# Kernel tuning notes

Hardware: AMD Instinct MI355X
Metric: run time of the kernel (lower is better)

The kernel has to match this reference:

```python
import jax, jax.numpy as jnp
import numpy as np

AMPLITUDE_STD = 4.2  # repo constant (unexported); normalization scale for ln_mag
EPS = 1e-8


def _interp_bias(table, x):
    # Linear interpolation of a 1D table over frequency domain [-1, 1].
    n = table.shape[0]
    idx = jnp.clip((x + 1.0) * 0.5 * (n - 1), 0.0, float(n - 1))
    i0 = jnp.floor(idx).astype(jnp.int32)
    i1 = jnp.minimum(i0 + 1, n - 1)
    w = idx - i0.astype(idx.dtype)
    return table[i0] * (1.0 - w) + table[i1] * w


def setup_inputs() -> dict:
    key = jax.random.key(0)
    k1, k2, k3, k4 = jax.random.split(key, 4)
    B, F, P, W, H = 8, 128, 32, 96, 96
    return {
        "mode_shapes": jax.random.normal(k1, (B, 2, P, W, H), dtype=jnp.float32),
        "mode_responses": jax.random.normal(k2, (B, F, 2, P), dtype=jnp.float32),
        "freqs": jax.random.uniform(k3, (B, F), dtype=jnp.float32, minval=-1.0, maxval=1.0),
        "bias_table": jax.random.normal(k4, (250,), dtype=jnp.float32) * 0.1,
    }


def reference(mode_shapes, mode_responses, freqs, bias_table):
    B, _, P, W, H = mode_shapes.shape
    F = mode_responses.shape[1]
    # _normalize_mode: L2 norm over (real/imag, W, H) per (batch, peak)
    norm = jnp.sqrt(jnp.sum(mode_shapes ** 2, axis=(1, 3, 4)))  # (B,P)
    ms = mode_shapes / (norm[:, None, :, None, None] + EPS)
    s_r, s_i = ms[:, 0], ms[:, 1]                                # (B,P,W,H)
    t_r, t_i = mode_responses[:, :, 0], mode_responses[:, :, 1]  # (B,F,P)
    f = 1.0 / P
    # complex superposition over modes: contraction over n_peaks
    rr = jnp.einsum('bpwh,bfp->bfwh', s_r, t_r)
    ii = jnp.einsum('bpwh,bfp->bfwh', s_i, t_i)
    ri = jnp.einsum('bpwh,bfp->bfwh', s_r, t_i)
    ir = jnp.einsum('bpwh,bfp->bfwh', s_i, t_r)
    r_new = f * (rr - ii)  # (B,F,W,H)
    i_new = f * (ri + ir)
    mag2 = r_new ** 2 + i_new ** 2
    bias = _interp_bias(bias_table, freqs)                       # (B,F)
    ln_mag = (jnp.log(mag2 + EPS) + bias[:, :, None, None]) / AMPLITUDE_STD
    fnorm = jnp.sum(mag2, axis=(-1, -2), keepdims=True)
    fnorm = jnp.sqrt(jnp.clip(fnorm, jnp.finfo(fnorm.dtype).eps))
    normed_field = jnp.stack([r_new / fnorm, i_new / fnorm], axis=2)  # (B,F,2,W,H)
    # aux sparsity loss over mode responses
    mr = mode_responses.reshape(B, F * 2, P)
    aux_sparse = jnp.mean(jnp.mean(jnp.log(jnp.linalg.norm(mr, axis=1) + 1.0), axis=1))
    return ln_mag, normed_field, aux_sparse
```

## Files before the change

kernel.cpp:

```cpp
#include <hip/hip_runtime.h>
#include <hip/hip_bf16.h>
#include <math.h>

#define WHN 9216
#define PN 32
#define FN 128
#define BN 8
#define EPSF 1e-8f
#define INV_STD 0.23809523809f
#define AUX_IDX 28311552

typedef __attribute__((ext_vector_type(8))) short short8;
typedef __attribute__((ext_vector_type(16))) float f32x16;

__device__ __forceinline__ unsigned short bfbits(__hip_bfloat16 h) {
  return *reinterpret_cast<unsigned short*>(&h);
}

__device__ __forceinline__ unsigned int bfsplit_pk(float v) {
  __hip_bfloat16 h = __float2bfloat16(v);
  unsigned int hs = bfbits(h);
  float r = v - __bfloat162float(h);
  unsigned int ls = bfbits(__float2bfloat16(r));
  return hs | (ls << 16);
}

__global__ __launch_bounds__(256) void k_gram(const float* __restrict__ ms,
                                              float* __restrict__ wsM,
                                              float* __restrict__ wsA,
                                              float* __restrict__ part,
                                              int use_part) {
  const int b = blockIdx.y;
  const int chunk = blockIdx.x;
  const int tid = threadIdx.x;
  __shared__ float4 sA[32][32];
  __shared__ float4 sB[32][32];
  __shared__ float pbuf[2][2048];
  const float4* ms4 = (const float4*)ms;
#pragma unroll
  for (int k = 0; k < 4; ++k) {
    int i4 = tid + k * 256;
    int xq = i4 & 31, p = i4 >> 5;
    sA[xq][p ^ xq] = ms4[((b * 2 + 0) * 32 + p) * 2304 + chunk * 32 + xq];
    sB[xq][p ^ xq] = ms4[((b * 2 + 1) * 32 + p) * 2304 + chunk * 32 + xq];
  }
  __syncthreads();
  const int w = tid >> 6, lane = tid & 63;
  const int pg = lane & 7, qg = lane >> 3;
  float accM[4][4] = {{0}}, accA[4][4] = {{0}};
  for (int xq = w; xq < 32; xq += 4) {
    float4 pa[4], pb[4], qa[4], qb[4];
#pragma unroll
    for (int j = 0; j < 4; ++j) {
      pa[j] = sA[xq][(pg + 8 * j) ^ xq];
      pb[j] = sB[xq][(pg + 8 * j) ^ xq];
      qa[j] = sA[xq][(qg + 8 * j) ^ xq];
      qb[j] = sB[xq][(qg + 8 * j) ^ xq];
    }
#pragma unroll
    for (int j = 0; j < 4; ++j)
#pragma unroll
      for (int k = 0; k < 4; ++k) {
        accM[j][k] += pa[j].x * qa[k].x + pb[j].x * qb[k].x
                    + pa[j].y * qa[k].y + pb[j].y * qb[k].y
                    + pa[j].z * qa[k].z + pb[j].z * qb[k].z
                    + pa[j].w * qa[k].w + pb[j].w * qb[k].w;
        accA[j][k] += pa[j].x * qb[k].x - pb[j].x * qa[k].x
                    + pa[j].y * qb[k].y - pb[j].y * qa[k].y
                    + pa[j].z * qb[k].z - pb[j].z * qa[k].z
                    + pa[j].w * qb[k].w - pb[j].w * qa[k].w;
      }
  }
  if (w < 2) {
#pragma unroll
    for (int j = 0; j < 4; ++j)
#pragma unroll
      for (int k = 0; k < 4; ++k) {
        pbuf[w][lane * 32 + j * 4 + k] = accM[j][k];
        pbuf[w][lane * 32 + 16 + j * 4 + k] = accA[j][k];
      }
  }
  __syncthreads();
  if (w >= 2) {
#pragma unroll
    for (int j = 0; j < 4; ++j)
#pragma unroll
      for (int k = 0; k < 4; ++k) {
        pbuf[w - 2][lane * 32 + j * 4 + k] += accM[j][k];
        pbuf[w - 2][lane * 32 + 16 + j * 4 + k] += accA[j][k];
      }
  }
  __syncthreads();
  for (int idx = tid; idx < 2048; idx += 256) {
    float v = pbuf[0][idx] + pbuf[1][idx];
    if (use_part) {
      part[((size_t)(b * 72 + chunk)) * 2048 + idx] = v;
    } else {
      int lane2 = idx >> 5, r = idx & 31;
      int mat = r >> 4, rr = r & 15, j = rr >> 2, k = rr & 3;
      int p = (lane2 & 7) + 8 * j, q = (lane2 >> 3) + 8 * k;
      float* dst = mat ? wsA : wsM;
      atomicAdd(dst + (b << 10) + p * 32 + q, v);
    }
  }
}

__global__ __launch_bounds__(256) void k_mid(const float* __restrict__ part,
                                             float* __restrict__ wsM,
                                             float* __restrict__ wsA,
                                             float* __restrict__ wsc,
                                             float* __restrict__ out) {
  int g = blockIdx.x * 256 + threadIdx.x;
  if (g == 0) out[AUX_IDX] = 0.f;
  int b = g >> 11, idx = g & 2047;
  const float* p = part + ((size_t)b * 72) * 2048 + idx;
  float s = 0.f;
#pragma unroll 8
  for (int c = 0; c < 72; ++c) s += p[(size_t)c * 2048];
  int lane2 = idx >> 5, r = idx & 31;
  int mat = r >> 4, rr = r & 15, j = rr >> 2, k = rr & 3;
  int pp = (lane2 & 7) + 8 * j, q = (lane2 >> 3) + 8 * k;
  (mat ? wsA : wsM)[(b << 10) + pp * 32 + q] = s;
  if (!mat && pp == q) wsc[(b << 5) + pp] = (1.0f / 32.0f) / (sqrtf(s) + EPSF);
}

__global__ void k_cfromM(const float* __restrict__ wsM, float* __restrict__ wsc,
                         float* __restrict__ out) {
  int tid = threadIdx.x;
  if (tid == 0) out[AUX_IDX] = 0.f;
  int b = tid >> 5, p = tid & 31;
  float m = wsM[(b << 10) + p * 33];
  wsc[tid] = (1.0f / 32.0f) / (sqrtf(m) + EPSF);
}

__global__ __launch_bounds__(64) void k_fnb(const float* __restrict__ t,
                                            const float* __restrict__ freqs,
                                            const float* __restrict__ btab,
                                            const float* __restrict__ wsM,
                                            const float* __restrict__ wsA,
                                            const float* __restrict__ wsc,
                                            float* __restrict__ wsinv,
                                            float* __restrict__ wsbias,
                                            short* __restrict__ wsT,
                                            float* __restrict__ out) {
  const int lane = threadIdx.x;
  if (blockIdx.x >= 1032) {
    const int b = blockIdx.x - 1032;
    __shared__ float sc[32];
    if (lane < 32) sc[lane] = wsc[b * 32 + lane];
    __syncthreads();
    short* dstH = wsT + (size_t)b * 16384;
    short* dstL = dstH + 8192;
#pragma unroll 2
    for (int it = 0; it < 16; ++it) {
      int slot = it * 64 + lane;
      int fl = slot >> 3, g = slot & 7;
      const float* src = t + ((size_t)(b * 128 + fl) * 2 + (g >> 2)) * 32 + (g & 3) * 8;
      int gs = g ^ (fl & 7);
      short8 hv, lv;
#pragma unroll
      for (int e = 0; e < 8; ++e) {
        unsigned int pk = bfsplit_pk(src[e] * sc[(g & 3) * 8 + e]);
        hv[e] = (short)(pk & 0xFFFFu);
        lv[e] = (short)(pk >> 16);
      }
      *(short8*)&dstH[fl * 64 + gs * 8] = hv;
      *(short8*)&dstL[fl * 64 + gs * 8] = lv;
    }
    return;
  }
  if (blockIdx.x >= 1024) {
    const int b = blockIdx.x - 1024;
    const int p = lane & 31, comp = lane >> 5;
    float acc = 0.f;
#pragma unroll 4
    for (int f = 0; f < FN; ++f) {
      float v = t[((size_t)(b * FN + f) * 2 + comp) * PN + p];
      acc = fmaf(v, v, acc);
    }
    acc += __shfl_xor(acc, 32);
    float val = logf(sqrtf(acc) + 1.0f);
#pragma unroll
    for (int off = 1; off <= 16; off <<= 1) val += __shfl_xor(val, off);
    if (lane == 0) atomicAdd(out + AUX_IDX, val * (1.0f / 256.0f));
    return;
  }
  const int bf = blockIdx.x;
  const int b = bf >> 7;
  __shared__ float tt[64];
  {
    int p = lane & 31, comp = lane >> 5;
    tt[lane] = t[(bf * 2 + comp) * PN + p] * wsc[(b << 5) + p];
  }
  __syncthreads();
  const int pp = lane & 31, qh = lane >> 5;
  const float* Mrow = wsM + (b << 10) + pp * 32 + qh * 16;
  const float* Arow = wsA + (b << 10) + pp * 32 + qh * 16;
  float ap = tt[pp], bp = tt[32 + pp];
  float S = 0.f;
#pragma unroll
  for (int k = 0; k < 16; ++k) {
    int q = qh * 16 + k;
    float aq = tt[q], bq = tt[32 + q];
    S += (ap * aq + bp * bq) * Mrow[k] + 2.0f * (bp * aq) * Arow[k];
  }
#pragma unroll
  for (int off = 32; off; off >>= 1) S += __shfl_xor(S, off);
  if (lane == 0) {
    float fn = sqrtf(fmaxf(S, 1.1920929e-7f));
    wsinv[bf] = 1.0f / fn;
    float x = freqs[bf];
    float idx = (x + 1.0f) * 0.5f * 249.0f;
    idx = fminf(fmaxf(idx, 0.0f), 249.0f);
    float fi = floorf(idx);
    int i0 = (int)fi;
    int i1 = min(i0 + 1, 249);
    float wvv = idx - fi;
    wsbias[bf] = btab[i0] * (1.0f - wvv) + btab[i1] * wvv;
  }
}

#define MFMA32(A, B, C) __builtin_amdgcn_mfma_f32_32x32x16_bf16(A, B, C, 0, 0, 0)
__global__ __launch_bounds__(256, 2) void k_main(const float* __restrict__ ms,
                                                 const short* __restrict__ wsT,
                                                 const float* __restrict__ wsinv,
                                                 const float* __restrict__ wsbias,
                                                 float* __restrict__ out) {
  __shared__ short tHs[4096];
  __shared__ short tLs[4096];
  __shared__ float sInv[64], sBias[64];
  const int b = blockIdx.y;
  const int z = blockIdx.z;
  const int tid = threadIdx.x;
  const int lane = tid & 63, wv = tid >> 6;
  const int col = lane & 31, hf = lane >> 5;
  const int pix = blockIdx.x * 128 + wv * 32 + col;
  const int f0 = z * 64;

  {
    const short* gH = wsT + (size_t)b * 16384 + (size_t)z * 4096;
#pragma unroll
    for (int it = 0; it < 4; ++it) {
      int chunk = wv * 4 + it;
      int half = chunk >> 3;
      int off = (chunk & 7) * 512;
      const short* g = gH + half * 8192 + off + lane * 8;
      short* l = (half ? tLs : tHs) + off;
      __builtin_amdgcn_global_load_lds(
          (const __attribute__((address_space(1))) unsigned int*)g,
          (__attribute__((address_space(3))) unsigned int*)l, 16, 0, 0);
    }
  }

  const float* msb = ms + (size_t)b * 64 * WHN + pix;
  short8 sHf[4], sLf[4];
#pragma unroll
  for (int kg = 0; kg < 4; ++kg) {
#pragma unroll
    for (int j = 0; j < 8; ++j) {
      int k = kg * 16 + hf * 8 + j;
      unsigned int pk = bfsplit_pk(msb[(size_t)k * WHN]);
      sHf[kg][j] = (short)(pk & 0xFFFFu);
      sLf[kg][j] = (short)(pk >> 16);
    }
  }
  short8 msk;
#pragma unroll
  for (int j = 0; j < 8; ++j) msk[j] = (short)0x8000;
  short8 nH2 = sHf[2] ^ msk, nL2 = sLf[2] ^ msk;
  short8 nH3 = sHf[3] ^ msk, nL3 = sLf[3] ^ msk;

  if (tid < 64) sInv[tid] = wsinv[b * 128 + f0 + tid];
  else if (tid < 128) sBias[tid - 64] = wsbias[b * 128 + f0 + (tid - 64)];
  __syncthreads();

  float* outF = out + (size_t)BN * FN * WHN;

#pragma unroll
  for (int ft = 0; ft < 2; ++ft) {
    short8 tHf[4], tLf[4];
    int fl = ft * 32 + col;
    int fx = fl & 7;
#pragma unroll
    for (int kg = 0; kg < 4; ++kg) {
      int gs = (2 * kg + hf) ^ fx;
      tHf[kg] = *(const short8*)&tHs[fl * 64 + gs * 8];
      tLf[kg] = *(const short8*)&tLs[fl * 64 + gs * 8];
    }
    f32x16 aR, aI;
#pragma unroll
    for (int i = 0; i < 16; ++i) { aR[i] = 0.f; aI[i] = 0.f; }
    aR = MFMA32(tHf[0], sHf[0], aR); aR = MFMA32(tHf[0], sLf[0], aR); aR = MFMA32(tLf[0], sHf[0], aR);
    aR = MFMA32(tHf[1], sHf[1], aR); aR = MFMA32(tHf[1], sLf[1], aR); aR = MFMA32(tLf[1], sHf[1], aR);
    aR = MFMA32(tHf[2], nH2,    aR); aR = MFMA32(tHf[2], nL2,    aR); aR = MFMA32(tLf[2], nH2,    aR);
    aR = MFMA32(tHf[3], nH3,    aR); aR = MFMA32(tHf[3], nL3,    aR); aR = MFMA32(tLf[3], nH3,    aR);
    aI = MFMA32(tHf[0], sHf[2], aI); aI = MFMA32(tHf[0], sLf[2], aI); aI = MFMA32(tLf[0], sHf[2], aI);
    aI = MFMA32(tHf[1], sHf[3], aI); aI = MFMA32(tHf[1], sLf[3], aI); aI = MFMA32(tLf[1], sHf[3], aI);
    aI = MFMA32(tHf[2], sHf[0], aI); aI = MFMA32(tHf[2], sLf[0], aI); aI = MFMA32(tLf[2], sHf[0], aI);
    aI = MFMA32(tHf[3], sHf[1], aI); aI = MFMA32(tHf[3], sLf[1], aI); aI = MFMA32(tLf[3], sHf[1], aI);
#pragma unroll
    for (int r = 0; r < 16; ++r) {
      int row = (r & 3) + 8 * (r >> 2) + 4 * hf;
      int fo = ft * 32 + row;
      float vr = aR[r], vi = aI[r];
      float mag2 = fmaf(vr, vr, vi * vi);
      float ln = (__logf(mag2 + EPSF) + sBias[fo]) * INV_STD;
      float inv = sInv[fo];
      size_t fg = (size_t)(b * 128 + f0 + fo);
      __builtin_nontemporal_store(ln, out + fg * WHN + pix);
      __builtin_nontemporal_store(vr * inv, outF + (fg * 2) * WHN + pix);
      __builtin_nontemporal_store(vi * inv, outF + (fg * 2 + 1) * WHN + pix);
    }
  }
}

extern "C" void kernel_launch(void* const* d_in, const int* in_sizes, int n_in,
                              void* d_out, int out_size, void* d_ws, size_t ws_size,
                              hipStream_t stream) {
  const float* ms = (const float*)d_in[0];
  const float* t  = (const float*)d_in[1];
  const float* fr = (const float*)d_in[2];
  const float* bt = (const float*)d_in[3];
  float* out = (float*)d_out;
  float* ws = (float*)d_ws;
  float* wsM = ws;
  float* wsA = ws + 8192;
  float* wsc = ws + 16384;
  float* wsinv = ws + 16640;
  float* wsbias = ws + 17664;
  float* part = ws + 18688;
  const size_t PART_FLOATS = (size_t)576 * 2048;
  size_t need = ((size_t)18688 + PART_FLOATS + 65536) * 4;
  int use_part = (ws_size >= need) ? 1 : 0;
  short* wsT = use_part ? (short*)(part + PART_FLOATS) : (short*)(ws + 18688);

  if (use_part) {
    hipLaunchKernelGGL(k_gram, dim3(72, 8), dim3(256), 0, stream, ms, wsM, wsA, part, 1);
    hipLaunchKernelGGL(k_mid, dim3(64), dim3(256), 0, stream, part, wsM, wsA, wsc, out);
  } else {
    (void)hipMemsetAsync(ws, 0, 16384 * sizeof(float), stream);
    hipLaunchKernelGGL(k_gram, dim3(72, 8), dim3(256), 0, stream, ms, wsM, wsA, part, 0);
    hipLaunchKernelGGL(k_cfromM, dim3(1), dim3(256), 0, stream, wsM, wsc, out);
  }
  hipLaunchKernelGGL(k_fnb, dim3(1040), dim3(64), 0, stream, t, fr, bt, wsM, wsA, wsc, wsinv, wsbias, wsT, out);
  hipLaunchKernelGGL(k_main, dim3(72, 8, 2), dim3(256), 0, stream, ms, wsT, wsinv, wsbias, out);
}
```

Before: 167.2 us.

## Fuse gram, reduction, prep and main stages into one cooperative persistent kernel

Replaces the four-kernel launch sequence with a single cooperative kernel that runs the Gram partials, the partial reduction, the per-frequency norm/bias/transpose prep, and the MFMA output stage as phases of one launch, separated by grid-wide syncs. Blocks loop persistently over tiles, and the main phase reloads the LDS tile only when the batch/half index changes. The goal is to remove kernel launch gaps and tail effects between the small stages. In exchange it adds grid.sync costs, a grid capped at 512 blocks that may lower occupancy for the main output phase, and host-side device and occupancy queries on every call.

```diff
diff --git a/kernel.cpp b/kernel.cpp
--- a/kernel.cpp
+++ b/kernel.cpp
@@ -1,6 +1,9 @@
 #include <hip/hip_runtime.h>
 #include <hip/hip_bf16.h>
+#include <hip/hip_cooperative_groups.h>
 #include <math.h>
+
+namespace cg = cooperative_groups;
 
 #define WHN 9216
 #define PN 32
@@ -23,6 +26,271 @@
   float r = v - __bfloat162float(h);
   unsigned int ls = bfbits(__float2bfloat16(r));
   return hs | (ls << 16);
+}
+
+#define MFMA32(A, B, C) __builtin_amdgcn_mfma_f32_32x32x16_bf16(A, B, C, 0, 0, 0)
+
+__global__ __launch_bounds__(256, 2) void k_fused(
+    const float* __restrict__ ms, const float* __restrict__ t,
+    const float* __restrict__ freqs, const float* __restrict__ btab,
+    float* __restrict__ ws, float* __restrict__ out) {
+  cg::grid_group grid = cg::this_grid();
+  __shared__ __align__(16) char smem[49152];
+  float* wsM = ws;
+  float* wsA = ws + 8192;
+  float* wsc = ws + 16384;
+  float* wsinv = ws + 16640;
+  float* wsbias = ws + 17664;
+  float* part = ws + 18688;
+  short* wsT = (short*)(part + (size_t)576 * 2048);
+
+  const int blk = blockIdx.x, tid = threadIdx.x;
+  const int lane = tid & 63, wv = tid >> 6;
+
+  {
+    float4* sA = (float4*)smem;
+    float4* sB = (float4*)(smem + 16384);
+    float* pbuf = (float*)(smem + 32768);
+    const float4* ms4 = (const float4*)ms;
+    for (int tIdx = blk; tIdx < 576; tIdx += gridDim.x) {
+      if (tIdx != blk) __syncthreads();
+      const int b = tIdx & 7, chunk = tIdx >> 3;
+#pragma unroll
+      for (int k = 0; k < 4; ++k) {
+        int i4 = tid + k * 256;
+        int xq = i4 & 31, p = i4 >> 5;
+        sA[xq * 32 + (p ^ xq)] = ms4[((b * 2 + 0) * 32 + p) * 2304 + chunk * 32 + xq];
+        sB[xq * 32 + (p ^ xq)] = ms4[((b * 2 + 1) * 32 + p) * 2304 + chunk * 32 + xq];
+      }
+      __syncthreads();
+      const int pg = lane & 7, qg = lane >> 3;
+      float accM[4][4] = {{0}}, accA[4][4] = {{0}};
+      for (int xq = wv; xq < 32; xq += 4) {
+        float4 pa[4], pb[4], qa[4], qb[4];
+#pragma unroll
+        for (int j = 0; j < 4; ++j) {
+          pa[j] = sA[xq * 32 + ((pg + 8 * j) ^ xq)];
+          pb[j] = sB[xq * 32 + ((pg + 8 * j) ^ xq)];
+          qa[j] = sA[xq * 32 + ((qg + 8 * j) ^ xq)];
+          qb[j] = sB[xq * 32 + ((qg + 8 * j) ^ xq)];
+        }
+#pragma unroll
+        for (int j = 0; j < 4; ++j)
+#pragma unroll
+          for (int k = 0; k < 4; ++k) {
+            accM[j][k] += pa[j].x * qa[k].x + pb[j].x * qb[k].x
+                        + pa[j].y * qa[k].y + pb[j].y * qb[k].y
+                        + pa[j].z * qa[k].z + pb[j].z * qb[k].z
+                        + pa[j].w * qa[k].w + pb[j].w * qb[k].w;
+            accA[j][k] += pa[j].x * qb[k].x - pb[j].x * qa[k].x
+                        + pa[j].y * qb[k].y - pb[j].y * qa[k].y
+                        + pa[j].z * qb[k].z - pb[j].z * qa[k].z
+                        + pa[j].w * qb[k].w - pb[j].w * qa[k].w;
+          }
+      }
+      if (wv < 2) {
+#pragma unroll
+        for (int j = 0; j < 4; ++j)
+#pragma unroll
+          for (int k = 0; k < 4; ++k) {
+            pbuf[wv * 2048 + lane * 32 + j * 4 + k] = accM[j][k];
+            pbuf[wv * 2048 + lane * 32 + 16 + j * 4 + k] = accA[j][k];
+          }
+      }
+      __syncthreads();
+      if (wv >= 2) {
+#pragma unroll
+        for (int j = 0; j < 4; ++j)
+#pragma unroll
+          for (int k = 0; k < 4; ++k) {
+            pbuf[(wv - 2) * 2048 + lane * 32 + j * 4 + k] += accM[j][k];
+            pbuf[(wv - 2) * 2048 + lane * 32 + 16 + j * 4 + k] += accA[j][k];
+          }
+      }
+      __syncthreads();
+      for (int idx = tid; idx < 2048; idx += 256)
+        part[(size_t)tIdx * 2048 + idx] = pbuf[idx] + pbuf[2048 + idx];
+    }
+  }
+  __threadfence();
+  grid.sync();
+
+  {
+    if (blk == 0 && tid == 0) out[AUX_IDX] = 0.f;
+    for (int g = blk * 256 + tid; g < 16384; g += gridDim.x * 256) {
+      int b = g >> 11, idx = g & 2047;
+      const float* p = part + (size_t)b * 2048 + idx;
+      float s = 0.f;
+#pragma unroll 8
+      for (int c = 0; c < 72; ++c) s += p[(size_t)c * 16384];
+      int lane2 = idx >> 5, r = idx & 31;
+      int mat = r >> 4, rr = r & 15, j = rr >> 2, k2 = rr & 3;
+      int pp = (lane2 & 7) + 8 * j, q = (lane2 >> 3) + 8 * k2;
+      (mat ? wsA : wsM)[(b << 10) + pp * 32 + q] = s;
+      if (!mat && pp == q) wsc[(b << 5) + pp] = (1.0f / 32.0f) / (sqrtf(s) + EPSF);
+    }
+  }
+  __threadfence();
+  grid.sync();
+
+  {
+    const int nw = gridDim.x * 4;
+    for (int task = blk * 4 + wv; task < 1032; task += nw) {
+      if (task < 1024) {
+        const int bf = task, b = bf >> 7;
+        const int p = lane & 31, comp = lane >> 5;
+        float tval = t[(bf * 2 + comp) * PN + p] * wsc[(b << 5) + p];
+        const int pp = lane & 31, qh = lane >> 5;
+        const float* Mrow = wsM + (b << 10) + pp * 32 + qh * 16;
+        const float* Arow = wsA + (b << 10) + pp * 32 + qh * 16;
+        float ap = __shfl(tval, pp);
+        float bp = __shfl(tval, 32 + pp);
+        float S = 0.f;
+#pragma unroll
+        for (int k = 0; k < 16; ++k) {
+          int q = qh * 16 + k;
+          float aq = __shfl(tval, q);
+          float bq = __shfl(tval, 32 + q);
+          S += (ap * aq + bp * bq) * Mrow[k] + 2.0f * (bp * aq) * Arow[k];
+        }
+#pragma unroll
+        for (int off = 32; off; off >>= 1) S += __shfl_xor(S, off);
+        if (lane == 0) {
+          float fn = sqrtf(fmaxf(S, 1.1920929e-7f));
+          wsinv[bf] = 1.0f / fn;
+          float x = freqs[bf];
+          float idx = (x + 1.0f) * 0.5f * 249.0f;
+          idx = fminf(fmaxf(idx, 0.0f), 249.0f);
+          float fi = floorf(idx);
+          int i0 = (int)fi;
+          int i1 = min(i0 + 1, 249);
+          float wvv = idx - fi;
+          wsbias[bf] = btab[i0] * (1.0f - wvv) + btab[i1] * wvv;
+        }
+      } else {
+        const int b = task - 1024;
+        const int p = lane & 31, comp = lane >> 5;
+        float acc = 0.f;
+#pragma unroll 4
+        for (int f = 0; f < FN; ++f) {
+          float v = t[((size_t)(b * FN + f) * 2 + comp) * PN + p];
+          acc = fmaf(v, v, acc);
+        }
+        acc += __shfl_xor(acc, 32);
+        float val = logf(sqrtf(acc) + 1.0f);
+#pragma unroll
+        for (int off = 1; off <= 16; off <<= 1) val += __shfl_xor(val, off);
+        if (lane == 0) atomicAdd(out + AUX_IDX, val * (1.0f / 256.0f));
+      }
+    }
+    for (int g2 = blk * 256 + tid; g2 < 8192; g2 += gridDim.x * 256) {
+      int b = g2 >> 10, slot = g2 & 1023;
+      int fl = slot >> 3, g = slot & 7;
+      const float* src = t + ((size_t)(b * 128 + fl) * 2 + (g >> 2)) * 32 + (g & 3) * 8;
+      int gs = g ^ (fl & 7);
+      short8 hv, lv;
+#pragma unroll
+      for (int e = 0; e < 8; ++e) {
+        unsigned int pk = bfsplit_pk(src[e] * wsc[b * 32 + (g & 3) * 8 + e]);
+        hv[e] = (short)(pk & 0xFFFFu);
+        lv[e] = (short)(pk >> 16);
+      }
+      short* dstH = wsT + (size_t)b * 16384;
+      *(short8*)&dstH[fl * 64 + gs * 8] = hv;
+      *(short8*)&dstH[8192 + fl * 64 + gs * 8] = lv;
+    }
+  }
+  __threadfence();
+  grid.sync();
+
+  {
+    short* tHs = (short*)smem;
+    short* tLs = (short*)(smem + 8192);
+    float* sInv = (float*)(smem + 16384);
+    float* sBias = (float*)(smem + 16640);
+    const int col = lane & 31, hf = lane >> 5;
+    float* outF = out + (size_t)BN * FN * WHN;
+    short8 msk;
+#pragma unroll
+    for (int j = 0; j < 8; ++j) msk[j] = (short)0x8000;
+
+    int last_bz = -1;
+    for (int tIdx = blk; tIdx < 1152; tIdx += gridDim.x) {
+      const int bz = tIdx & 15, c = tIdx >> 4;
+      const int b = bz >> 1, z = bz & 1, f0 = z * 64;
+      if (bz != last_bz) {
+        __syncthreads();
+        const short* gH = wsT + (size_t)b * 16384 + (size_t)z * 4096;
+#pragma unroll
+        for (int it = 0; it < 4; ++it) {
+          int chunk2 = wv * 4 + it;
+          int half = chunk2 >> 3;
+          int off = (chunk2 & 7) * 512;
+          const short* gsrc = gH + half * 8192 + off + lane * 8;
+          short* l = (half ? tLs : tHs) + off;
+          __builtin_amdgcn_global_load_lds(
+              (const __attribute__((address_space(1))) unsigned int*)gsrc,
+              (__attribute__((address_space(3))) unsigned int*)l, 16, 0, 0);
+        }
+        if (tid < 64) sInv[tid] = wsinv[b * 128 + f0 + tid];
+        else if (tid < 128) sBias[tid - 64] = wsbias[b * 128 + f0 + (tid - 64)];
+        __syncthreads();
+        last_bz = bz;
+      }
+      const int pix = c * 128 + wv * 32 + col;
+      const float* msb = ms + (size_t)b * 64 * WHN + pix;
+      short8 sHf[4], sLf[4];
+#pragma unroll
+      for (int kg = 0; kg < 4; ++kg) {
+#pragma unroll
+        for (int j = 0; j < 8; ++j) {
+          int k = kg * 16 + hf * 8 + j;
+          unsigned int pk = bfsplit_pk(msb[(size_t)k * WHN]);
+          sHf[kg][j] = (short)(pk & 0xFFFFu);
+          sLf[kg][j] = (short)(pk >> 16);
+        }
+      }
+      short8 nH2 = sHf[2] ^ msk, nL2 = sLf[2] ^ msk;
+      short8 nH3 = sHf[3] ^ msk, nL3 = sLf[3] ^ msk;
+
+#pragma unroll
+      for (int ft = 0; ft < 2; ++ft) {
+        short8 tHf[4], tLf[4];
+        int fl = ft * 32 + col;
+        int fx = fl & 7;
+#pragma unroll
+        for (int kg = 0; kg < 4; ++kg) {
+          int gs = (2 * kg + hf) ^ fx;
+          tHf[kg] = *(const short8*)&tHs[fl * 64 + gs * 8];
+          tLf[kg] = *(const short8*)&tLs[fl * 64 + gs * 8];
+        }
+        f32x16 aR, aI;
+#pragma unroll
+        for (int i = 0; i < 16; ++i) { aR[i] = 0.f; aI[i] = 0.f; }
+        aR = MFMA32(tHf[0], sHf[0], aR); aR = MFMA32(tHf[0], sLf[0], aR); aR = MFMA32(tLf[0], sHf[0], aR);
+        aR = MFMA32(tHf[1], sHf[1], aR); aR = MFMA32(tHf[1], sLf[1], aR); aR = MFMA32(tLf[1], sHf[1], aR);
+        aR = MFMA32(tHf[2], nH2,    aR); aR = MFMA32(tHf[2], nL2,    aR); aR = MFMA32(tLf[2], nH2,    aR);
+        aR = MFMA32(tHf[3], nH3,    aR); aR = MFMA32(tHf[3], nL3,    aR); aR = MFMA32(tLf[3], nH3,    aR);
+        aI = MFMA32(tHf[0], sHf[2], aI); aI = MFMA32(tHf[0], sLf[2], aI); aI = MFMA32(tLf[0], sHf[2], aI);
+        aI = MFMA32(tHf[1], sHf[3], aI); aI = MFMA32(tHf[1], sLf[3], aI); aI = MFMA32(tLf[1], sHf[3], aI);
+        aI = MFMA32(tHf[2], sHf[0], aI); aI = MFMA32(tHf[2], sLf[0], aI); aI = MFMA32(tLf[2], sHf[0], aI);
+        aI = MFMA32(tHf[3], sHf[1], aI); aI = MFMA32(tHf[3], sLf[1], aI); aI = MFMA32(tLf[3], sHf[1], aI);
+#pragma unroll
+        for (int r = 0; r < 16; ++r) {
+          int row = (r & 3) + 8 * (r >> 2) + 4 * hf;
+          int fo = ft * 32 + row;
+          float vr = aR[r], vi = aI[r];
+          float mag2 = fmaf(vr, vr, vi * vi);
+          float ln = (__logf(mag2 + EPSF) + sBias[fo]) * INV_STD;
+          float inv = sInv[fo];
+          size_t fg = (size_t)(b * 128 + f0 + fo);
+          __builtin_nontemporal_store(ln, out + fg * WHN + pix);
+          __builtin_nontemporal_store(vr * inv, outF + (fg * 2) * WHN + pix);
+          __builtin_nontemporal_store(vi * inv, outF + (fg * 2 + 1) * WHN + pix);
+        }
+      }
+    }
+  }
 }
 
 __global__ __launch_bounds__(256) void k_gram(const float* __restrict__ ms,
@@ -220,7 +488,6 @@
   }
 }
 
-#define MFMA32(A, B, C) __builtin_amdgcn_mfma_f32_32x32x16_bf16(A, B, C, 0, 0, 0)
 __global__ __launch_bounds__(256, 2) void k_main(const float* __restrict__ ms,
                                                  const short* __restrict__ wsT,
                                                  const float* __restrict__ wsinv,
@@ -236,7 +503,6 @@
   const int col = lane & 31, hf = lane >> 5;
   const int pix = blockIdx.x * 128 + wv * 32 + col;
   const int f0 = z * 64;
-
   {
     const short* gH = wsT + (size_t)b * 16384 + (size_t)z * 4096;
 #pragma unroll
@@ -251,7 +517,6 @@
           (__attribute__((address_space(3))) unsigned int*)l, 16, 0, 0);
     }
   }
-
   const float* msb = ms + (size_t)b * 64 * WHN + pix;
   short8 sHf[4], sLf[4];
 #pragma unroll
@@ -269,13 +534,10 @@
   for (int j = 0; j < 8; ++j) msk[j] = (short)0x8000;
   short8 nH2 = sHf[2] ^ msk, nL2 = sLf[2] ^ msk;
   short8 nH3 = sHf[3] ^ msk, nL3 = sLf[3] ^ msk;
-
   if (tid < 64) sInv[tid] = wsinv[b * 128 + f0 + tid];
-  else if (tid < 128) sBias[tid - 64] = wsbias[b * 128 + f0 + (tid - 64)];
+  else if (tid < 128) sBias[tid - 64] = wsbias[b * 128 + (tid - 64) + f0];
   __syncthreads();
-
   float* outF = out + (size_t)BN * FN * WHN;
-
 #pragma unroll
   for (int ft = 0; ft < 2; ++ft) {
     short8 tHf[4], tLf[4];
@@ -334,6 +596,27 @@
   int use_part = (ws_size >= need) ? 1 : 0;
   short* wsT = use_part ? (short*)(part + PART_FLOATS) : (short*)(ws + 18688);
 
+  int grid = 0;
+  if (use_part) {
+    int dev = 0;
+    if (hipGetDevice(&dev) == hipSuccess) {
+      int coop = 0, nCU = 0, occ = 0;
+      (void)hipDeviceGetAttribute(&coop, hipDeviceAttributeCooperativeLaunch, dev);
+      (void)hipDeviceGetAttribute(&nCU, hipDeviceAttributeMultiprocessorCount, dev);
+      (void)hipOccupancyMaxActiveBlocksPerMultiprocessor(&occ, k_fused, 256, 0);
+      if (coop && nCU > 0 && occ > 0) {
+        int g = occ * nCU;
+        if (g > 512) g = 512;
+        grid = g & ~15;
+      }
+    }
+  }
+  if (grid >= 16) {
+    void* args[] = {(void*)&ms, (void*)&t, (void*)&fr, (void*)&bt, (void*)&ws, (void*)&out};
+    (void)hipLaunchCooperativeKernel(k_fused, dim3(grid), dim3(256), args, 0, stream);
+    return;
+  }
+
   if (use_part) {
     hipLaunchKernelGGL(k_gram, dim3(72, 8), dim3(256), 0, stream, ms, wsM, wsA, part, 1);
     hipLaunchKernelGGL(k_mid, dim3(64), dim3(256), 0, stream, part, wsM, wsA, wsc, out);
```

New measurement: 355.5 us. 2.13x slower.
